# Performance work log

Measured on AMD Instinct MI355X. Metric: run time of the kernel, lower is better.

## Reference

```python
import jax, jax.numpy as jnp
import numpy as np

N, E, G, H, D, O, L = 200000, 800000, 8192, 128, 32, 256, 3
NODE_VOCABS = [119, 9, 11, 12, 9, 5, 8, 2, 2]
EDGE_VOCABS = [22, 6, 2]


def setup_inputs() -> dict:
    key = jax.random.key(0)
    ks = jax.random.split(key, 40)
    rn = lambda k, shape: jax.random.normal(k, shape, jnp.float32) * 0.05
    inp = {
        "x": jax.random.randint(ks[0], (N, 9), 0, 2, jnp.int32),
        "edge_attr": jax.random.randint(ks[1], (E, 3), 0, 2, jnp.int32),
        "edge_index": jax.random.randint(ks[2], (2, E), 0, N, jnp.int32),
        "batch_ids": jnp.sort(jax.random.randint(ks[3], (N,), 0, G, jnp.int32)),
    }
    for i, v in enumerate(NODE_VOCABS):
        inp[f"emb{i}"] = rn(ks[4 + i], (v, D))
    inp["node_w"] = rn(ks[13], (9 * D, H)); inp["node_b"] = jnp.zeros((H,), jnp.float32)
    inp["ebond"] = rn(ks[14], (EDGE_VOCABS[0], D))
    inp["estereo"] = rn(ks[15], (EDGE_VOCABS[1], D))
    inp["econj"] = rn(ks[16], (EDGE_VOCABS[2], D))
    inp["edge_w"] = rn(ks[17], (3 * D, H)); inp["edge_b"] = jnp.zeros((H,), jnp.float32)
    inp["conv_w1"] = rn(ks[18], (L, H, H)); inp["conv_b1"] = jnp.zeros((L, H), jnp.float32)
    inp["conv_w2"] = rn(ks[19], (L, H, H)); inp["conv_b2"] = jnp.zeros((L, H), jnp.float32)
    inp["proj_w"] = rn(ks[20], (H, O)); inp["proj_b"] = jnp.zeros((O,), jnp.float32)
    return inp


def reference(x, edge_attr, edge_index, batch_ids,
              emb0, emb1, emb2, emb3, emb4, emb5, emb6, emb7, emb8,
              node_w, node_b, ebond, estereo, econj, edge_w, edge_b,
              conv_w1, conv_b1, conv_w2, conv_b2, proj_w, proj_b):
    node_tabs = [emb0, emb1, emb2, emb3, emb4, emb5, emb6, emb7, emb8]
    # node feature embedding concat -> [N, 9*D] -> project to hidden
    h = jnp.concatenate([t[x[:, i]] for i, t in enumerate(node_tabs)], axis=-1)
    h = h @ node_w + node_b  # [N, H]
    # edge feature embedding concat -> project to hidden
    e = jnp.concatenate([ebond[edge_attr[:, 0]], estereo[edge_attr[:, 1]],
                         econj[edge_attr[:, 2]]], axis=-1)
    e = e @ edge_w + edge_b  # [E, H]

    src, dst = edge_index[0], edge_index[1]
    for l in range(L):
        # GINEConv (eps=0): out = MLP(x_i + sum_j relu(x_j + e_ji))
        msg = jax.nn.relu(h[src] + e)                              # [E, H]
        agg = jax.ops.segment_sum(msg, dst, num_segments=N)        # [N, H]
        z = (h + agg) @ conv_w1[l] + conv_b1[l]
        z = jax.nn.relu(z) @ conv_w2[l] + conv_b2[l]
        h = jax.nn.relu(z)  # outer ReLU from forward loop

    g = jax.ops.segment_sum(h, batch_ids, num_segments=G)  # global_add_pool [G, H]
    g = g @ proj_w + proj_b                                 # [G, O]
    # F.normalize(dim=-1): x / max(||x||2, 1e-12)
    g = g / jnp.maximum(jnp.linalg.norm(g, axis=-1, keepdims=True), 1e-12)
    return g
```

## Files before the change

### kernel.cpp

```cpp
#include <hip/hip_runtime.h>
#include <hip/hip_bf16.h>

#define NN 200000
#define NE 800000
#define NG 8192
#define HD 128
#define OD 256

typedef __attribute__((ext_vector_type(8))) short bf16x8;
typedef __attribute__((ext_vector_type(4))) float f32x4;
typedef __attribute__((ext_vector_type(2))) float f32x2;

__device__ inline unsigned short f2bf(float x) {
    unsigned u = __float_as_uint(x);
    unsigned r = u + 0x7FFFu + ((u >> 16) & 1u);
    return (unsigned short)(r >> 16);
}
__device__ inline float b2f(unsigned short u) {
    return __uint_as_float((unsigned)u << 16);
}
__device__ inline f32x2 up2(unsigned u) {
    f32x2 r;
    r.x = __uint_as_float(u << 16);
    r.y = __uint_as_float(u & 0xFFFF0000u);
    return r;
}

__global__ void init_kernel(int* __restrict__ deg, int* __restrict__ gstart, int* __restrict__ gend) {
    int idx = blockIdx.x * 256 + threadIdx.x;
    if (idx < NN) deg[idx] = 0;
    if (idx < NG) { gstart[idx] = NN; gend[idx] = 0; }
}

__global__ void setup_kernel(
    const float* __restrict__ e0, const float* __restrict__ e1, const float* __restrict__ e2,
    const float* __restrict__ e3, const float* __restrict__ e4, const float* __restrict__ e5,
    const float* __restrict__ e6, const float* __restrict__ e7, const float* __restrict__ e8,
    const float* __restrict__ node_w, const float* __restrict__ node_b,
    const float* __restrict__ ebond, const float* __restrict__ estereo, const float* __restrict__ econj,
    const float* __restrict__ edge_w, const float* __restrict__ edge_b,
    const float* __restrict__ cw1, const float* __restrict__ cw2,
    float* __restrict__ P, float* __restrict__ T, unsigned short* __restrict__ Wt)
{
    int idx = blockIdx.x * 256 + threadIdx.x;
    const int NP = 177 * 128;
    const int NT = NP + 30 * 128;
    if (idx < NP) {
        int row = idx >> 7, j = idx & 127;
        const int offs[10] = {0,119,128,139,151,160,165,173,175,177};
        int i = 0;
        while (row >= offs[i+1]) ++i;
        int lv = row - offs[i];
        const float* emb;
        switch (i) {
            case 0: emb = e0; break; case 1: emb = e1; break; case 2: emb = e2; break;
            case 3: emb = e3; break; case 4: emb = e4; break; case 5: emb = e5; break;
            case 6: emb = e6; break; case 7: emb = e7; break; default: emb = e8; break;
        }
        float acc = (i == 0) ? node_b[j] : 0.f;
        const float* wcol = node_w + (i * 32) * 128 + j;
        #pragma unroll
        for (int d = 0; d < 32; ++d) acc += emb[lv*32 + d] * wcol[d*128];
        P[idx] = acc;
    } else if (idx < NT) {
        int k = idx - NP;
        int row = k >> 7, j = k & 127;
        int i, lv; const float* emb;
        if (row < 22)      { i = 0; lv = row;      emb = ebond;   }
        else if (row < 28) { i = 1; lv = row - 22; emb = estereo; }
        else               { i = 2; lv = row - 28; emb = econj;   }
        float acc = (i == 0) ? edge_b[j] : 0.f;
        const float* wcol = edge_w + (i * 32) * 128 + j;
        #pragma unroll
        for (int d = 0; d < 32; ++d) acc += emb[lv*32 + d] * wcol[d*128];
        T[k] = acc;
    } else if (idx < NT + 6 * 16384) {
        int w = idx - NT;
        int m = w >> 14;
        int rem = w & 16383;
        int j = rem >> 7, k = rem & 127;
        int l = m >> 1;
        const float* W = ((m & 1) ? cw2 : cw1) + (size_t)l * 16384;
        Wt[w] = f2bf(W[k * 128 + j]);
    }
}

__global__ __launch_bounds__(256) void combine_embed_kernel(
    const float* __restrict__ T, unsigned short* __restrict__ Tcb,
    const int* __restrict__ x, const float* __restrict__ P, unsigned short* __restrict__ h)
{
    if (blockIdx.x < 132) {
        int idx = blockIdx.x * 256 + threadIdx.x;
        if (idx >= 264 * 128) return;
        int row = idx >> 7, j = idx & 127;
        int a0 = row / 12, rem = row % 12;
        int a1 = rem >> 1, a2 = rem & 1;
        Tcb[idx] = f2bf(T[a0 * 128 + j] + T[(22 + a1) * 128 + j] + T[(28 + a2) * 128 + j]);
        return;
    }
    int g = threadIdx.x >> 5, lane = threadIdx.x & 31;
    int n = (blockIdx.x - 132) * 8 + g;
    const int offs[9] = {0,119,128,139,151,160,165,173,175};
    int c4 = lane * 4;
    float ax = 0.f, ay = 0.f, az = 0.f, aw = 0.f;
    #pragma unroll
    for (int i = 0; i < 9; ++i) {
        int xv = x[n*9 + i];
        float4 p = *(const float4*)&P[(offs[i] + xv) * 128 + c4];
        ax += p.x; ay += p.y; az += p.z; aw += p.w;
    }
    ushort4 o = {f2bf(ax), f2bf(ay), f2bf(az), f2bf(aw)};
    *(ushort4*)&h[(size_t)n*128 + c4] = o;
}

__global__ void hist_bounds_kernel(const int* __restrict__ dst, int* __restrict__ deg,
                                   const int* __restrict__ bid,
                                   int* __restrict__ gstart, int* __restrict__ gend) {
    if (blockIdx.x < NE / 256) {
        int e = blockIdx.x * 256 + threadIdx.x;
        atomicAdd(&deg[dst[e]], 1);
        return;
    }
    int idx = (blockIdx.x - NE / 256) * 256 + threadIdx.x;
    if (idx < NN) {
        int b = bid[idx];
        atomicMin(&gstart[b], idx);
        atomicMax(&gend[b], idx + 1);
    }
}

__global__ void scan_block_sum(const int* __restrict__ deg, int* __restrict__ partial) {
    __shared__ int sm[256];
    int idx = blockIdx.x * 256 + threadIdx.x;
    int v = (idx < NN) ? deg[idx] : 0;
    sm[threadIdx.x] = v; __syncthreads();
    for (int off = 128; off > 0; off >>= 1) {
        if (threadIdx.x < off) sm[threadIdx.x] += sm[threadIdx.x + off];
        __syncthreads();
    }
    if (threadIdx.x == 0) partial[blockIdx.x] = sm[0];
}

__global__ void scan_partials(int* __restrict__ partial, int nb) {
    __shared__ int sm[1024];
    int t = threadIdx.x;
    int v = (t < nb) ? partial[t] : 0;
    sm[t] = v; __syncthreads();
    for (int off = 1; off < 1024; off <<= 1) {
        int xv = (t >= off) ? sm[t - off] : 0;
        __syncthreads();
        sm[t] += xv;
        __syncthreads();
    }
    if (t < nb) partial[t] = sm[t] - v;
}

__global__ void scan_finalize(const int* __restrict__ deg, const int* __restrict__ partial,
                              int* __restrict__ start, int* __restrict__ cursor) {
    __shared__ int sm[256];
    int t = threadIdx.x;
    int idx = blockIdx.x * 256 + t;
    int v = (idx < NN) ? deg[idx] : 0;
    sm[t] = v; __syncthreads();
    for (int off = 1; off < 256; off <<= 1) {
        int xv = (t >= off) ? sm[t - off] : 0;
        __syncthreads();
        sm[t] += xv;
        __syncthreads();
    }
    int excl = sm[t] - v + partial[blockIdx.x];
    if (idx < NN) {
        start[idx] = excl;
        cursor[idx] = excl;
        if (idx == NN - 1) start[NN] = excl + v;
    }
}

__global__ void scatter_kernel(const int* __restrict__ src, const int* __restrict__ dst,
                               const int* __restrict__ eattr, int* __restrict__ cursor,
                               int2* __restrict__ csr) {
    int e = blockIdx.x * 256 + threadIdx.x;
    int d = dst[e];
    int p = atomicAdd(&cursor[d], 1);
    int a0 = eattr[e*3], a1 = eattr[e*3+1], a2 = eattr[e*3+2];
    csr[p] = make_int2(src[e] << 8, (a0 * 12 + a1 * 2 + a2) << 8);
}

__global__ __launch_bounds__(256) void agg_kernel(
    const unsigned short* __restrict__ h, const unsigned short* __restrict__ Tcb,
    const int* __restrict__ start, const int2* __restrict__ csr,
    unsigned short* __restrict__ s)
{
    int g = threadIdx.x >> 4, lane = threadIdx.x & 15;
    int n = blockIdx.x * 16 + g;
    int st = start[n], en = start[n + 1];
    int lb = lane * 16;
    const char* hb = (const char*)h;
    const char* tb = (const char*)Tcb;
    const f32x2 zero = {0.f, 0.f};
    f32x2 a0 = zero, a1 = zero, a2 = zero, a3 = zero;
    f32x2 c0 = zero, c1 = zero, c2 = zero, c3 = zero;
    int p = st;
    for (; p + 2 <= en; p += 2) {
        int2 ea = csr[p];
        int2 eb = csr[p + 1];
        uint4 hv0 = *(const uint4*)(hb + ea.x + lb);
        uint4 tv0 = *(const uint4*)(tb + ea.y + lb);
        uint4 hv1 = *(const uint4*)(hb + eb.x + lb);
        uint4 tv1 = *(const uint4*)(tb + eb.y + lb);
        a0 += __builtin_elementwise_max(up2(hv0.x) + up2(tv0.x), zero);
        a1 += __builtin_elementwise_max(up2(hv0.y) + up2(tv0.y), zero);
        a2 += __builtin_elementwise_max(up2(hv0.z) + up2(tv0.z), zero);
        a3 += __builtin_elementwise_max(up2(hv0.w) + up2(tv0.w), zero);
        c0 += __builtin_elementwise_max(up2(hv1.x) + up2(tv1.x), zero);
        c1 += __builtin_elementwise_max(up2(hv1.y) + up2(tv1.y), zero);
        c2 += __builtin_elementwise_max(up2(hv1.z) + up2(tv1.z), zero);
        c3 += __builtin_elementwise_max(up2(hv1.w) + up2(tv1.w), zero);
    }
    if (p < en) {
        int2 ea = csr[p];
        uint4 hv0 = *(const uint4*)(hb + ea.x + lb);
        uint4 tv0 = *(const uint4*)(tb + ea.y + lb);
        a0 += __builtin_elementwise_max(up2(hv0.x) + up2(tv0.x), zero);
        a1 += __builtin_elementwise_max(up2(hv0.y) + up2(tv0.y), zero);
        a2 += __builtin_elementwise_max(up2(hv0.z) + up2(tv0.z), zero);
        a3 += __builtin_elementwise_max(up2(hv0.w) + up2(tv0.w), zero);
    }
    uint4 hn = *(const uint4*)(hb + (size_t)n * 256 + lb);
    f32x2 r0 = up2(hn.x) + a0 + c0;
    f32x2 r1 = up2(hn.y) + a1 + c1;
    f32x2 r2 = up2(hn.z) + a2 + c2;
    f32x2 r3 = up2(hn.w) + a3 + c3;
    uint4 o;
    o.x = (unsigned)f2bf(r0.x) | ((unsigned)f2bf(r0.y) << 16);
    o.y = (unsigned)f2bf(r1.x) | ((unsigned)f2bf(r1.y) << 16);
    o.z = (unsigned)f2bf(r2.x) | ((unsigned)f2bf(r2.y) << 16);
    o.w = (unsigned)f2bf(r3.x) | ((unsigned)f2bf(r3.y) << 16);
    *(uint4*)((char*)s + (size_t)n * 256 + lb) = o;
}

__global__ __launch_bounds__(256) void mlp_mfma_kernel(
    const unsigned short* __restrict__ sin, unsigned short* __restrict__ hout,
    const unsigned short* __restrict__ W1t, const float* __restrict__ b1,
    const unsigned short* __restrict__ W2t, const float* __restrict__ b2)
{
    __shared__ unsigned short tile[64 * 128];
    int tid = threadIdx.x;
    int r0 = blockIdx.x * 64;
    int wave = tid >> 6, lane = tid & 63;
    int q = lane >> 4, lr = lane & 15;
    int wcol0 = wave * 32;

    #pragma unroll
    for (int it = 0; it < 4; ++it) {
        int cid = it * 256 + tid;
        int r = cid >> 4, c = cid & 15;
        bf16x8 v = *(const bf16x8*)&sin[(size_t)(r0 + r) * 128 + c * 8];
        int chunk = c ^ (r & 7);
        *(bf16x8*)&tile[r * 128 + chunk * 8] = v;
    }

    bf16x8 Bf[4][2];
    #pragma unroll
    for (int ct = 0; ct < 2; ++ct) {
        #pragma unroll
        for (int ks = 0; ks < 4; ++ks)
            Bf[ks][ct] = *(const bf16x8*)&W1t[(size_t)(wcol0 + ct * 16 + lr) * 128 + ks * 32 + q * 8];
    }
    float bv[2];
    bv[0] = b1[wcol0 + lr];
    bv[1] = b1[wcol0 + 16 + lr];

    __syncthreads();

    f32x4 acc[4][2];
    #pragma unroll
    for (int rt = 0; rt < 4; ++rt)
        #pragma unroll
        for (int ct = 0; ct < 2; ++ct)
            acc[rt][ct] = (f32x4){0.f, 0.f, 0.f, 0.f};
    #pragma unroll
    for (int ks = 0; ks < 4; ++ks) {
        #pragma unroll
        for (int rt = 0; rt < 4; ++rt) {
            bf16x8 A = *(const bf16x8*)&tile[(rt * 16 + lr) * 128 + (((ks * 4 + q) ^ (lr & 7)) * 8)];
            #pragma unroll
            for (int ct = 0; ct < 2; ++ct)
                acc[rt][ct] = __builtin_amdgcn_mfma_f32_16x16x32_bf16(A, Bf[ks][ct], acc[rt][ct], 0, 0, 0);
        }
    }

    __syncthreads();

    #pragma unroll
    for (int ct = 0; ct < 2; ++ct) {
        #pragma unroll
        for (int ks = 0; ks < 4; ++ks)
            Bf[ks][ct] = *(const bf16x8*)&W2t[(size_t)(wcol0 + ct * 16 + lr) * 128 + ks * 32 + q * 8];
    }

    #pragma unroll
    for (int rt = 0; rt < 4; ++rt) {
        #pragma unroll
        for (int ct = 0; ct < 2; ++ct) {
            int col = wcol0 + ct * 16 + lr;
            int chunkc = col >> 3, cl = col & 7;
            #pragma unroll
            for (int i = 0; i < 4; ++i) {
                int row = rt * 16 + q * 4 + i;
                float z = fmaxf(acc[rt][ct][i] + bv[ct], 0.f);
                tile[row * 128 + ((chunkc ^ (row & 7)) * 8) + cl] = f2bf(z);
            }
        }
    }

    bv[0] = b2[wcol0 + lr];
    bv[1] = b2[wcol0 + 16 + lr];

    __syncthreads();

    #pragma unroll
    for (int rt = 0; rt < 4; ++rt)
        #pragma unroll
        for (int ct = 0; ct < 2; ++ct)
            acc[rt][ct] = (f32x4){0.f, 0.f, 0.f, 0.f};
    #pragma unroll
    for (int ks = 0; ks < 4; ++ks) {
        #pragma unroll
        for (int rt = 0; rt < 4; ++rt) {
            bf16x8 A = *(const bf16x8*)&tile[(rt * 16 + lr) * 128 + (((ks * 4 + q) ^ (lr & 7)) * 8)];
            #pragma unroll
            for (int ct = 0; ct < 2; ++ct)
                acc[rt][ct] = __builtin_amdgcn_mfma_f32_16x16x32_bf16(A, Bf[ks][ct], acc[rt][ct], 0, 0, 0);
        }
    }

    __syncthreads();

    #pragma unroll
    for (int rt = 0; rt < 4; ++rt) {
        #pragma unroll
        for (int ct = 0; ct < 2; ++ct) {
            int col = wcol0 + ct * 16 + lr;
            int chunkc = col >> 3, cl = col & 7;
            #pragma unroll
            for (int i = 0; i < 4; ++i) {
                int row = rt * 16 + q * 4 + i;
                float o = fmaxf(acc[rt][ct][i] + bv[ct], 0.f);
                tile[row * 128 + ((chunkc ^ (row & 7)) * 8) + cl] = f2bf(o);
            }
        }
    }

    __syncthreads();

    #pragma unroll
    for (int it = 0; it < 4; ++it) {
        int cid = it * 256 + tid;
        int r = cid >> 4, c = cid & 15;
        bf16x8 v = *(const bf16x8*)&tile[r * 128 + ((c ^ (r & 7)) * 8)];
        *(bf16x8*)&hout[(size_t)(r0 + r) * 128 + c * 8] = v;
    }
}

__global__ __launch_bounds__(256) void pool_kernel(
    const unsigned short* __restrict__ h, const int* __restrict__ gstart, const int* __restrict__ gend,
    const float* __restrict__ pw, const float* __restrict__ pb, float* __restrict__ out)
{
    __shared__ float pooled[128];
    __shared__ float red[1024];
    int g = blockIdx.x, t = threadIdx.x;
    int gs = gstart[g], ge = gend[g];
    int lane = t & 31, half = t >> 5;
    int c4 = lane * 4;
    float ax = 0.f, ay = 0.f, az = 0.f, aw = 0.f;
    for (int r = gs + half; r < ge; r += 8) {
        ushort4 v = *(const ushort4*)&h[(size_t)r * 128 + c4];
        ax += b2f(v.x); ay += b2f(v.y); az += b2f(v.z); aw += b2f(v.w);
    }
    red[t*4+0] = ax; red[t*4+1] = ay; red[t*4+2] = az; red[t*4+3] = aw;
    __syncthreads();
    if (half < 4) {
        #pragma unroll
        for (int i = 0; i < 4; ++i) red[t*4+i] += red[(t+128)*4+i];
    }
    __syncthreads();
    if (half < 2) {
        #pragma unroll
        for (int i = 0; i < 4; ++i) red[t*4+i] += red[(t+64)*4+i];
    }
    __syncthreads();
    if (half < 1) {
        #pragma unroll
        for (int i = 0; i < 4; ++i) pooled[c4+i] = red[t*4+i] + red[(t+32)*4+i];
    }
    __syncthreads();
    float acc = pb[t];
    for (int k = 0; k < 128; ++k) acc += pooled[k] * pw[k * 256 + t];
    red[t] = acc * acc; __syncthreads();
    for (int off = 128; off > 0; off >>= 1) {
        if (t < off) red[t] += red[t + off];
        __syncthreads();
    }
    float nrm = sqrtf(red[0]);
    float scale = 1.f / fmaxf(nrm, 1e-12f);
    out[g * 256 + t] = acc * scale;
}

extern "C" void kernel_launch(void* const* d_in, const int* in_sizes, int n_in,
                              void* d_out, int out_size, void* d_ws, size_t ws_size,
                              hipStream_t stream) {
    const int* x     = (const int*)d_in[0];
    const int* eattr = (const int*)d_in[1];
    const int* eidx  = (const int*)d_in[2];
    const int* bids  = (const int*)d_in[3];
    const float* emb0 = (const float*)d_in[4];
    const float* emb1 = (const float*)d_in[5];
    const float* emb2 = (const float*)d_in[6];
    const float* emb3 = (const float*)d_in[7];
    const float* emb4 = (const float*)d_in[8];
    const float* emb5 = (const float*)d_in[9];
    const float* emb6 = (const float*)d_in[10];
    const float* emb7 = (const float*)d_in[11];
    const float* emb8 = (const float*)d_in[12];
    const float* node_w = (const float*)d_in[13];
    const float* node_b = (const float*)d_in[14];
    const float* ebond   = (const float*)d_in[15];
    const float* estereo = (const float*)d_in[16];
    const float* econj   = (const float*)d_in[17];
    const float* edge_w  = (const float*)d_in[18];
    const float* edge_b  = (const float*)d_in[19];
    const float* conv_w1 = (const float*)d_in[20];
    const float* conv_b1 = (const float*)d_in[21];
    const float* conv_w2 = (const float*)d_in[22];
    const float* conv_b2 = (const float*)d_in[23];
    const float* proj_w  = (const float*)d_in[24];
    const float* proj_b  = (const float*)d_in[25];
    float* out = (float*)d_out;

    char* ws = (char*)d_ws;
    size_t off = 0;
    auto alloc = [&](size_t bytes) -> void* {
        void* p = ws + off;
        off += (bytes + 255) / 256 * 256;
        return p;
    };
    unsigned short* h = (unsigned short*)alloc((size_t)NN * HD * 2);
    unsigned short* s = (unsigned short*)alloc((size_t)NN * HD * 2);
    float* P      = (float*)alloc(177 * 128 * 4);
    float* T      = (float*)alloc(30 * 128 * 4);
    unsigned short* Tcb = (unsigned short*)alloc(264 * 128 * 2);
    unsigned short* Wt = (unsigned short*)alloc(6 * 16384 * 2);
    int*   deg    = (int*)alloc((size_t)NN * 4);
    int*   start  = (int*)alloc((size_t)(NN + 1) * 4);
    int*   cursor = (int*)alloc((size_t)NN * 4);
    int*   partial= (int*)alloc(1024 * 4);
    int2*  csr    = (int2*)alloc((size_t)NE * 8);
    int*   gstart = (int*)alloc((size_t)NG * 4);
    int*   gend   = (int*)alloc((size_t)NG * 4);

    const int NB = (NN + 255) / 256;

    init_kernel<<<NB, 256, 0, stream>>>(deg, gstart, gend);
    setup_kernel<<<(26496 + 6 * 16384 + 255) / 256, 256, 0, stream>>>(
        emb0, emb1, emb2, emb3, emb4, emb5, emb6, emb7, emb8,
        node_w, node_b, ebond, estereo, econj, edge_w, edge_b,
        conv_w1, conv_w2, P, T, Wt);
    combine_embed_kernel<<<132 + NN / 8, 256, 0, stream>>>(T, Tcb, x, P, h);

    const int* srcp = eidx;
    const int* dstp = eidx + NE;
    hist_bounds_kernel<<<NE / 256 + NB, 256, 0, stream>>>(dstp, deg, bids, gstart, gend);
    scan_block_sum<<<NB, 256, 0, stream>>>(deg, partial);
    scan_partials<<<1, 1024, 0, stream>>>(partial, NB);
    scan_finalize<<<NB, 256, 0, stream>>>(deg, partial, start, cursor);
    scatter_kernel<<<NE / 256, 256, 0, stream>>>(srcp, dstp, eattr, cursor, csr);

    for (int l = 0; l < 3; ++l) {
        agg_kernel<<<NN / 16, 256, 0, stream>>>(h, Tcb, start, csr, s);
        mlp_mfma_kernel<<<NN / 64, 256, 0, stream>>>(s, h,
            Wt + (size_t)(l * 2) * 16384, conv_b1 + (size_t)l * HD,
            Wt + (size_t)(l * 2 + 1) * 16384, conv_b2 + (size_t)l * HD);
    }
    pool_kernel<<<NG, 256, 0, stream>>>(h, gstart, gend, proj_w, proj_b, out);
}
```

Before: 443.3 us.

## Degree-sort aggregation nodes, pre-swizzle agg output, direct-to-LDS MLP tile load

Nodes are binned by in-degree (capped at 31) through counting-sort bins built during the CSR scan, and agg_kernel walks nodes in that order so the 16 nodes in a block have similar degree and waste less time waiting on the longest one. agg_kernel now writes its output already XOR-swizzled, which lets mlp_mfma_kernel load its tile with global_load_lds straight into LDS instead of going through registers. Graph start/end bounds now come from neighbour comparisons on the sorted batch ids rather than atomics. The costs are a scattered ord[] lookup with irregular output writes in aggregation, and extra atomic and binning work in the scan kernels.

```diff
diff --git a/kernel.cpp b/kernel.cpp
--- a/kernel.cpp
+++ b/kernel.cpp
@@ -26,10 +26,12 @@
     return r;
 }
 
-__global__ void init_kernel(int* __restrict__ deg, int* __restrict__ gstart, int* __restrict__ gend) {
+__global__ void init_kernel(int* __restrict__ deg, int* __restrict__ gstart, int* __restrict__ gend,
+                            int* __restrict__ bin_total) {
     int idx = blockIdx.x * 256 + threadIdx.x;
     if (idx < NN) deg[idx] = 0;
     if (idx < NG) { gstart[idx] = NN; gend[idx] = 0; }
+    if (idx < 32) bin_total[idx] = 0;
 }
 
 __global__ void setup_kernel(
@@ -124,26 +126,38 @@
     int idx = (blockIdx.x - NE / 256) * 256 + threadIdx.x;
     if (idx < NN) {
         int b = bid[idx];
-        atomicMin(&gstart[b], idx);
-        atomicMax(&gend[b], idx + 1);
-    }
-}
-
-__global__ void scan_block_sum(const int* __restrict__ deg, int* __restrict__ partial) {
+        if (idx == 0 || bid[idx - 1] != b) gstart[b] = idx;
+        if (idx == NN - 1 || bid[idx + 1] != b) gend[b] = idx + 1;
+    }
+}
+
+__global__ void scan_block_sum(const int* __restrict__ deg, int* __restrict__ partial,
+                               int* __restrict__ bin_total) {
     __shared__ int sm[256];
-    int idx = blockIdx.x * 256 + threadIdx.x;
+    __shared__ int bc[32];
+    int t = threadIdx.x;
+    int idx = blockIdx.x * 256 + t;
     int v = (idx < NN) ? deg[idx] : 0;
-    sm[threadIdx.x] = v; __syncthreads();
+    sm[t] = v;
+    if (t < 32) bc[t] = 0;
+    __syncthreads();
+    if (idx < NN) atomicAdd(&bc[v > 31 ? 31 : v], 1);
     for (int off = 128; off > 0; off >>= 1) {
-        if (threadIdx.x < off) sm[threadIdx.x] += sm[threadIdx.x + off];
+        if (t < off) sm[t] += sm[t + off];
         __syncthreads();
     }
-    if (threadIdx.x == 0) partial[blockIdx.x] = sm[0];
-}
-
-__global__ void scan_partials(int* __restrict__ partial, int nb) {
+    if (t == 0) partial[blockIdx.x] = sm[0];
+    if (t < 32) atomicAdd(&bin_total[t], bc[t]);
+}
+
+__global__ void scan_partials(int* __restrict__ partial, int nb,
+                              const int* __restrict__ bin_total, int* __restrict__ bin_cursor) {
     __shared__ int sm[1024];
     int t = threadIdx.x;
+    if (t == 0) {
+        int r = 0;
+        for (int i = 0; i < 32; ++i) { int c = bin_total[i]; bin_cursor[i] = r; r += c; }
+    }
     int v = (t < nb) ? partial[t] : 0;
     sm[t] = v; __syncthreads();
     for (int off = 1; off < 1024; off <<= 1) {
@@ -156,12 +170,20 @@
 }
 
 __global__ void scan_finalize(const int* __restrict__ deg, const int* __restrict__ partial,
-                              int* __restrict__ start, int* __restrict__ cursor) {
+                              int* __restrict__ start, int* __restrict__ cursor,
+                              int* __restrict__ bin_cursor, int* __restrict__ ord) {
     __shared__ int sm[256];
+    __shared__ int bc[32];
+    __shared__ int bbase[32];
     int t = threadIdx.x;
     int idx = blockIdx.x * 256 + t;
     int v = (idx < NN) ? deg[idx] : 0;
-    sm[t] = v; __syncthreads();
+    sm[t] = v;
+    if (t < 32) bc[t] = 0;
+    __syncthreads();
+    int bin = v > 31 ? 31 : v;
+    int rank = 0;
+    if (idx < NN) rank = atomicAdd(&bc[bin], 1);
     for (int off = 1; off < 256; off <<= 1) {
         int xv = (t >= off) ? sm[t - off] : 0;
         __syncthreads();
@@ -174,6 +196,9 @@
         cursor[idx] = excl;
         if (idx == NN - 1) start[NN] = excl + v;
     }
+    if (t < 32) bbase[t] = atomicAdd(&bin_cursor[t], bc[t]);
+    __syncthreads();
+    if (idx < NN) ord[bbase[bin] + rank] = idx;
 }
 
 __global__ void scatter_kernel(const int* __restrict__ src, const int* __restrict__ dst,
@@ -189,10 +214,11 @@
 __global__ __launch_bounds__(256) void agg_kernel(
     const unsigned short* __restrict__ h, const unsigned short* __restrict__ Tcb,
     const int* __restrict__ start, const int2* __restrict__ csr,
+    const int* __restrict__ ord,
     unsigned short* __restrict__ s)
 {
     int g = threadIdx.x >> 4, lane = threadIdx.x & 15;
-    int n = blockIdx.x * 16 + g;
+    int n = ord[blockIdx.x * 16 + g];
     int st = start[n], en = start[n + 1];
     int lb = lane * 16;
     const char* hb = (const char*)h;
@@ -236,7 +262,7 @@
     o.y = (unsigned)f2bf(r1.x) | ((unsigned)f2bf(r1.y) << 16);
     o.z = (unsigned)f2bf(r2.x) | ((unsigned)f2bf(r2.y) << 16);
     o.w = (unsigned)f2bf(r3.x) | ((unsigned)f2bf(r3.y) << 16);
-    *(uint4*)((char*)s + (size_t)n * 256 + lb) = o;
+    *(uint4*)((char*)s + (size_t)n * 256 + ((lane ^ (n & 7)) * 16)) = o;
 }
 
 __global__ __launch_bounds__(256) void mlp_mfma_kernel(
@@ -244,20 +270,24 @@
     const unsigned short* __restrict__ W1t, const float* __restrict__ b1,
     const unsigned short* __restrict__ W2t, const float* __restrict__ b2)
 {
-    __shared__ unsigned short tile[64 * 128];
+    __shared__ __attribute__((aligned(16))) unsigned short tile[64 * 128];
     int tid = threadIdx.x;
     int r0 = blockIdx.x * 64;
     int wave = tid >> 6, lane = tid & 63;
     int q = lane >> 4, lr = lane & 15;
     int wcol0 = wave * 32;
 
-    #pragma unroll
-    for (int it = 0; it < 4; ++it) {
-        int cid = it * 256 + tid;
-        int r = cid >> 4, c = cid & 15;
-        bf16x8 v = *(const bf16x8*)&sin[(size_t)(r0 + r) * 128 + c * 8];
-        int chunk = c ^ (r & 7);
-        *(bf16x8*)&tile[r * 128 + chunk * 8] = v;
+    {
+        const char* sb = (const char*)sin + (size_t)r0 * 256;
+        char* tbb = (char*)tile;
+        #pragma unroll
+        for (int it = 0; it < 4; ++it) {
+            int base = (it * 256 + wave * 64) * 16;
+            __builtin_amdgcn_global_load_lds(
+                (const __attribute__((address_space(1))) void*)(sb + base + lane * 16),
+                (__attribute__((address_space(3))) void*)(tbb + base),
+                16, 0, 0);
+        }
     }
 
     bf16x8 Bf[4][2];
@@ -458,10 +488,13 @@
     int2*  csr    = (int2*)alloc((size_t)NE * 8);
     int*   gstart = (int*)alloc((size_t)NG * 4);
     int*   gend   = (int*)alloc((size_t)NG * 4);
+    int*   bin_total  = (int*)alloc(32 * 4);
+    int*   bin_cursor = (int*)alloc(32 * 4);
+    int*   ord    = (int*)alloc((size_t)NN * 4);
 
     const int NB = (NN + 255) / 256;
 
-    init_kernel<<<NB, 256, 0, stream>>>(deg, gstart, gend);
+    init_kernel<<<NB, 256, 0, stream>>>(deg, gstart, gend, bin_total);
     setup_kernel<<<(26496 + 6 * 16384 + 255) / 256, 256, 0, stream>>>(
         emb0, emb1, emb2, emb3, emb4, emb5, emb6, emb7, emb8,
         node_w, node_b, ebond, estereo, econj, edge_w, edge_b,
@@ -471,13 +504,13 @@
     const int* srcp = eidx;
     const int* dstp = eidx + NE;
     hist_bounds_kernel<<<NE / 256 + NB, 256, 0, stream>>>(dstp, deg, bids, gstart, gend);
-    scan_block_sum<<<NB, 256, 0, stream>>>(deg, partial);
-    scan_partials<<<1, 1024, 0, stream>>>(partial, NB);
-    scan_finalize<<<NB, 256, 0, stream>>>(deg, partial, start, cursor);
+    scan_block_sum<<<NB, 256, 0, stream>>>(deg, partial, bin_total);
+    scan_partials<<<1, 1024, 0, stream>>>(partial, NB, bin_total, bin_cursor);
+    scan_finalize<<<NB, 256, 0, stream>>>(deg, partial, start, cursor, bin_cursor, ord);
     scatter_kernel<<<NE / 256, 256, 0, stream>>>(srcp, dstp, eattr, cursor, csr);
 
     for (int l = 0; l < 3; ++l) {
-        agg_kernel<<<NN / 16, 256, 0, stream>>>(h, Tcb, start, csr, s);
+        agg_kernel<<<NN / 16, 256, 0, stream>>>(h, Tcb, start, csr, ord, s);
         mlp_mfma_kernel<<<NN / 64, 256, 0, stream>>>(s, h,
             Wt + (size_t)(l * 2) * 16384, conv_b1 + (size_t)l * HD,
             Wt + (size_t)(l * 2 + 1) * 16384, conv_b2 + (size_t)l * HD);
```

Measured after the change: 439.5 us. About the same (-0.9%).
